# Performance work log

Measured on AMD Instinct MI355X. Metric: run time of the kernel, lower is better.

Reference implementation:

```python
import jax, jax.numpy as jnp
import numpy as np

FLOW_NUM = 2048
H = 64  # lstm_output_dim
NOISE_DIM = 3


def _w(key, shape, s=0.08):
    return (jax.random.normal(key, shape, dtype=jnp.float32) * s)


def setup_inputs() -> dict:
    key = jax.random.key(0)
    ks = jax.random.split(key, 20)
    d = {
        "noise": jax.random.normal(ks[0], (FLOW_NUM, NOISE_DIM), dtype=jnp.float32),
        "w_ih0": _w(ks[1], (4 * H, NOISE_DIM)),
        "w_hh0": _w(ks[2], (4 * H, H)),
        "b_ih0": _w(ks[3], (4 * H,)),
        "b_hh0": _w(ks[4], (4 * H,)),
        "w_ih1": _w(ks[5], (4 * H, H)),
        "w_hh1": _w(ks[6], (4 * H, H)),
        "b_ih1": _w(ks[7], (4 * H,)),
        "b_hh1": _w(ks[8], (4 * H,)),
        "w_ih2": _w(ks[9], (4 * H, H)),
        "w_hh2": _w(ks[10], (4 * H, H)),
        "b_ih2": _w(ks[11], (4 * H,)),
        "b_hh2": _w(ks[12], (4 * H,)),
        "fc1_w": _w(ks[13], (32, H)),
        "fc1_b": _w(ks[14], (32,)),
        "fc2_w": _w(ks[15], (16, 32)),
        "fc2_b": _w(ks[16], (16,)),
        "fc3_w": _w(ks[17], (3, 16)),
        "fc3_b": _w(ks[18], (3,)),
        "flow_length": 500,
    }
    return d


def _lstm_cell(x, h, c, w_ih, w_hh, b_ih, b_hh):
    # PyTorch gate order: input, forget, cell(g), output
    gates = x @ w_ih.T + h @ w_hh.T + (b_ih + b_hh)
    i, f, g, o = jnp.split(gates, 4, axis=-1)
    c_new = jax.nn.sigmoid(f) * c + jax.nn.sigmoid(i) * jnp.tanh(g)
    h_new = jax.nn.sigmoid(o) * jnp.tanh(c_new)
    return h_new, c_new


def reference(noise, w_ih0, w_hh0, b_ih0, b_hh0,
              w_ih1, w_hh1, b_ih1, b_hh1,
              w_ih2, w_hh2, b_ih2, b_hh2,
              fc1_w, fc1_b, fc2_w, fc2_b, fc3_w, fc3_b,
              flow_length):
    layers = [(w_ih0, w_hh0, b_ih0, b_hh0),
              (w_ih1, w_hh1, b_ih1, b_hh1),
              (w_ih2, w_hh2, b_ih2, b_hh2)]
    n = noise.shape[0]
    h0 = jnp.zeros((3, n, H), dtype=noise.dtype)
    c0 = jnp.zeros((3, n, H), dtype=noise.dtype)

    def step(carry, _):
        x, h, c = carry
        inp = x
        hs, cs = [], []
        for l, (wi, wh, bi, bh) in enumerate(layers):
            h_l, c_l = _lstm_cell(inp, h[l], c[l], wi, wh, bi, bh)
            hs.append(h_l)
            cs.append(c_l)
            inp = h_l
        # MLP head (Dropout is identity in eval mode); LeakyReLU slope 0.01
        y = jax.nn.leaky_relu(inp @ fc1_w.T + fc1_b)
        y = jax.nn.leaky_relu(y @ fc2_w.T + fc2_b)
        y = jax.nn.leaky_relu(y @ fc3_w.T + fc3_b)
        return (y, jnp.stack(hs), jnp.stack(cs)), y

    _, flow = jax.lax.scan(step, (noise, h0, c0), None, length=flow_length)
    # flow: [flow_length, flow_num, 3] -> [flow_num, flow_length, 3]
    return jnp.swapaxes(flow, 0, 1)
```

## Files before the change

### kernel.cpp

```cpp
#include <hip/hip_runtime.h>

#define NT 512

typedef _Float16 f16x8 __attribute__((ext_vector_type(8)));
typedef _Float16 f16x4 __attribute__((ext_vector_type(4)));
typedef float    f32x4 __attribute__((ext_vector_type(4)));

#define MFMA(a, b, c) __builtin_amdgcn_mfma_f32_16x16x32_f16((a), (b), (c), 0, 0, 0)

#if __has_builtin(__builtin_amdgcn_exp2f)
__device__ __forceinline__ float fexp(float x) { return __builtin_amdgcn_exp2f(x * 1.4426950408889634f); }
#else
__device__ __forceinline__ float fexp(float x) { return __expf(x); }
#endif
#if __has_builtin(__builtin_amdgcn_rcpf)
__device__ __forceinline__ float frcp(float x) { return __builtin_amdgcn_rcpf(x); }
#else
__device__ __forceinline__ float frcp(float x) { return 1.0f / x; }
#endif
__device__ __forceinline__ float sigm(float x)  { return frcp(1.0f + fexp(-x)); }
__device__ __forceinline__ float tanh_(float x) { return 1.0f - 2.0f * frcp(1.0f + fexp(2.0f * x)); }
__device__ __forceinline__ float lrelu(float x) { return x > 0.0f ? x : 0.01f * x; }

__device__ __forceinline__ f16x8 ld8(const float* p) {
    const float4* q = (const float4*)p;
    float4 a = q[0], b = q[1];
    f16x8 r = { (_Float16)a.x, (_Float16)a.y, (_Float16)a.z, (_Float16)a.w,
                (_Float16)b.x, (_Float16)b.y, (_Float16)b.z, (_Float16)b.w };
    return r;
}

__device__ __forceinline__ f16x8 zero8() {
    f16x8 z;
#pragma unroll
    for (int i = 0; i < 8; ++i) z[i] = (_Float16)0.0f;
    return z;
}

__global__ __launch_bounds__(NT, 2)
void gen_kernel(
    const float* __restrict__ noise,
    const float* __restrict__ w_ih0, const float* __restrict__ w_hh0,
    const float* __restrict__ b_ih0, const float* __restrict__ b_hh0,
    const float* __restrict__ w_ih1, const float* __restrict__ w_hh1,
    const float* __restrict__ b_ih1, const float* __restrict__ b_hh1,
    const float* __restrict__ w_ih2, const float* __restrict__ w_hh2,
    const float* __restrict__ b_ih2, const float* __restrict__ b_hh2,
    const float* __restrict__ fc1_w, const float* __restrict__ fc1_b,
    const float* __restrict__ fc2_w, const float* __restrict__ fc2_b,
    const float* __restrict__ fc3_w, const float* __restrict__ fc3_b,
    const int*   __restrict__ flow_len_p,
    float* __restrict__ out)
{
    __shared__ _Float16 sh[3][16 * 64] __attribute__((aligned(16)));
    __shared__ _Float16 sy1[8][16][40] __attribute__((aligned(16)));
    __shared__ _Float16 sy2[8][16][40] __attribute__((aligned(16)));

    const int tid  = threadIdx.x;
    const int l    = tid & 63;
    const int w    = tid >> 6;
    const int ls   = l & 15;
    const int lj   = l >> 4;
    const int base = blockIdx.x * 8;
    const int T    = flow_len_p[0];

    const int gA  = ls & 3;
    const int rA0 = gA * 64 + 4 * (2 * w + 0) + (ls >> 2);
    const int rA1 = gA * 64 + 4 * (2 * w + 1) + (ls >> 2);

    f16x8 A1[2][4], A2[2][4], A0[2][3];
#pragma unroll
    for (int kc = 0; kc < 2; ++kc) {
        A1[0][kc]     = ld8(w_ih1 + rA0 * 64 + 32 * kc + 8 * lj);
        A1[1][kc]     = ld8(w_ih1 + rA1 * 64 + 32 * kc + 8 * lj);
        A1[0][2 + kc] = ld8(w_hh1 + rA0 * 64 + 32 * kc + 8 * lj);
        A1[1][2 + kc] = ld8(w_hh1 + rA1 * 64 + 32 * kc + 8 * lj);
        A2[0][kc]     = ld8(w_ih2 + rA0 * 64 + 32 * kc + 8 * lj);
        A2[1][kc]     = ld8(w_ih2 + rA1 * 64 + 32 * kc + 8 * lj);
        A2[0][2 + kc] = ld8(w_hh2 + rA0 * 64 + 32 * kc + 8 * lj);
        A2[1][2 + kc] = ld8(w_hh2 + rA1 * 64 + 32 * kc + 8 * lj);
        A0[0][kc]     = ld8(w_hh0 + rA0 * 64 + 32 * kc + 8 * lj);
        A0[1][kc]     = ld8(w_hh0 + rA1 * 64 + 32 * kc + 8 * lj);
    }
#pragma unroll
    for (int tt = 0; tt < 2; ++tt) {
        const int r = tt ? rA1 : rA0;
        f16x8 v;
#pragma unroll
        for (int i = 0; i < 8; ++i) {
            int kl = 8 * lj + i;
            float x = (kl < 3) ? w_ih0[r * 3 + kl]
                    : (kl == 3) ? (b_ih0[r] + b_hh0[r]) : 0.0f;
            v[i] = (_Float16)x;
        }
        A0[tt][2] = v;
    }
    f16x8 F1[2][2], F2, F3;
#pragma unroll
    for (int tt = 0; tt < 2; ++tt)
#pragma unroll
        for (int kc = 0; kc < 2; ++kc)
            F1[tt][kc] = ld8(fc1_w + (16 * tt + ls) * 64 + 32 * kc + 8 * lj);
    F2 = ld8(fc2_w + ls * 32 + 8 * lj);
    {
        f16x8 v;
#pragma unroll
        for (int i = 0; i < 8; ++i) {
            int k = 8 * lj + i;
            v[i] = (_Float16)((ls < 3 && k < 16) ? fc3_w[ls * 16 + k] : 0.0f);
        }
        F3 = v;
    }
    const int uc0 = 8 * w + lj, uc1 = 8 * w + 4 + lj;
    const int u_own = (ls < 8) ? uc0 : uc1;
    const int cs    = ls & 7;
    const int whaddr = cs * 64 + 8 * (((u_own >> 3) + cs) & 7) + (u_own & 7);
    float b1o[4], b2o[4];
#pragma unroll
    for (int g = 0; g < 4; ++g) {
        b1o[g] = b_ih1[g * 64 + u_own] + b_hh1[g * 64 + u_own];
        b2o[g] = b_ih2[g * 64 + u_own] + b_hh2[g * 64 + u_own];
    }
    float hb1a[4], hb1b[4], hb2[4];
#pragma unroll
    for (int r = 0; r < 4; ++r) {
        hb1a[r] = fc1_b[4 * lj + r];
        hb1b[r] = fc1_b[16 + 4 * lj + r];
        hb2[r]  = fc2_b[4 * lj + r];
    }
    float fb3[3] = { fc3_b[0], fc3_b[1], fc3_b[2] };

    for (int i = tid; i < 3 * 16 * 64; i += NT) ((_Float16*)sh)[i] = (_Float16)0.0f;
    for (int i = tid; i < 8 * 16 * 40; i += NT) {
        ((_Float16*)sy1)[i] = (_Float16)0.0f;
        ((_Float16*)sy2)[i] = (_Float16)0.0f;
    }
    __syncthreads();

    float c0s = 0.0f, c1s = 0.0f, c2s = 0.0f;
    const float zb[4] = {0, 0, 0, 0};

#define RD(L, kg) (*(const f16x8*)&sh[L][ls * 64 + 8 * (((kg) + ls) & 7)])

#define REPACK(cell, a0, a1)                                                   \
    float cell[4];                                                             \
    _Pragma("unroll")                                                          \
    for (int r = 0; r < 4; ++r) {                                              \
        float v_ = __shfl_xor(a1[r], 8);                                       \
        cell[r] = (ls < 8) ? a0[r] : v_;                                       \
    }

#define ACTC(cell, bo, cref, L) {                                              \
        float gi = cell[0] + bo[0], gf = cell[1] + bo[1];                      \
        float gg = cell[2] + bo[2], go = cell[3] + bo[3];                      \
        cref = sigm(gf) * cref + sigm(gi) * tanh_(gg);                         \
        sh[L][whaddr] = (_Float16)(sigm(go) * tanh_(cref)); }

    {
        f16x8 bx0 = zero8();
        if (lj == 0) {
            float n0 = 0.0f, n1 = 0.0f, n2 = 0.0f;
            if (ls < 8) {
                const float* np = noise + (size_t)(base + ls) * 3;
                n0 = np[0]; n1 = np[1]; n2 = np[2];
            }
            bx0[0] = (_Float16)n0; bx0[1] = (_Float16)n1;
            bx0[2] = (_Float16)n2; bx0[3] = (_Float16)1.0f;
        }
        f32x4 a0 = {0, 0, 0, 0}, a1 = {0, 0, 0, 0};
        a0 = MFMA(A0[0][2], bx0, a0);
        a1 = MFMA(A0[1][2], bx0, a1);
        REPACK(cell, a0, a1)
        ACTC(cell, zb, c0s, 0)
    }
    f16x8 h1r0 = zero8(), h1r1 = zero8();
    f16x8 h2r0 = zero8(), h2r1 = zero8();
    __syncthreads();

    for (int t = 0; t < T; ++t) {
        f16x8 r0 = RD(0, lj), r1 = RD(0, 4 + lj);
        {
            f32x4 u0 = {0,0,0,0}, u1 = {0,0,0,0}, v0 = {0,0,0,0}, v1 = {0,0,0,0};
            v0 = MFMA(A1[0][2], h1r0, v0); v1 = MFMA(A1[1][2], h1r0, v1);
            v0 = MFMA(A1[0][3], h1r1, v0); v1 = MFMA(A1[1][3], h1r1, v1);
            u0 = MFMA(A1[0][0], r0, u0);   u1 = MFMA(A1[1][0], r0, u1);
            u0 = MFMA(A1[0][1], r1, u0);   u1 = MFMA(A1[1][1], r1, u1);
            f32x4 a0 = u0 + v0, a1 = u1 + v1;
            REPACK(cell, a0, a1)
            ACTC(cell, b1o, c1s, 1)
        }
        __syncthreads();
        h1r0 = RD(1, lj); h1r1 = RD(1, 4 + lj);
        {
            f32x4 u0 = {0,0,0,0}, u1 = {0,0,0,0}, v0 = {0,0,0,0}, v1 = {0,0,0,0};
            v0 = MFMA(A2[0][2], h2r0, v0); v1 = MFMA(A2[1][2], h2r0, v1);
            v0 = MFMA(A2[0][3], h2r1, v0); v1 = MFMA(A2[1][3], h2r1, v1);
            u0 = MFMA(A2[0][0], h1r0, u0); u1 = MFMA(A2[1][0], h1r0, u1);
            u0 = MFMA(A2[0][1], h1r1, u0); u1 = MFMA(A2[1][1], h1r1, u1);
            f32x4 a0 = u0 + v0, a1 = u1 + v1;
            REPACK(cell, a0, a1)
            ACTC(cell, b2o, c2s, 2)
        }
        __syncthreads();
        h2r0 = RD(2, lj); h2r1 = RD(2, 4 + lj);
        {
            f32x4 h0a = {0,0,0,0}, h0b = {0,0,0,0};
            h0a = MFMA(A0[0][0], r0, h0a); h0b = MFMA(A0[1][0], r0, h0b);
            h0a = MFMA(A0[0][1], r1, h0a); h0b = MFMA(A0[1][1], r1, h0b);
            f32x4 y1a = {0,0,0,0}, y1b = {0,0,0,0};
            y1a = MFMA(F1[0][0], h2r0, y1a); y1b = MFMA(F1[1][0], h2r0, y1b);
            y1a = MFMA(F1[0][1], h2r1, y1a); y1b = MFMA(F1[1][1], h2r1, y1b);
            f16x4 vv;
#pragma unroll
            for (int r = 0; r < 4; ++r) vv[r] = (_Float16)lrelu(y1a[r] + hb1a[r]);
            *(f16x4*)&sy1[w][ls][4 * lj] = vv;
#pragma unroll
            for (int r = 0; r < 4; ++r) vv[r] = (_Float16)lrelu(y1b[r] + hb1b[r]);
            *(f16x4*)&sy1[w][ls][16 + 4 * lj] = vv;
            f16x8 by1 = *(const f16x8*)&sy1[w][ls][8 * lj];
            f32x4 y2 = {0,0,0,0};
            y2 = MFMA(F2, by1, y2);
#pragma unroll
            for (int r = 0; r < 4; ++r) vv[r] = (_Float16)lrelu(y2[r] + hb2[r]);
            *(f16x4*)&sy2[w][ls][4 * lj] = vv;
            f16x8 by2 = *(const f16x8*)&sy2[w][ls][8 * lj];
            f32x4 y3 = {0,0,0,0};
            y3 = MFMA(F3, by2, y3);
            f16x8 bx = zero8();
            if (lj == 0) {
                float o0 = lrelu(y3[0] + fb3[0]);
                float o1 = lrelu(y3[1] + fb3[1]);
                float o2 = lrelu(y3[2] + fb3[2]);
                bx[0] = (_Float16)o0; bx[1] = (_Float16)o1;
                bx[2] = (_Float16)o2; bx[3] = (_Float16)1.0f;
                if (w == 0 && ls < 8) {
                    float* op = out + ((size_t)(base + ls) * T + t) * 3;
                    op[0] = o0; op[1] = o1; op[2] = o2;
                }
            }
            h0a = MFMA(A0[0][2], bx, h0a);
            h0b = MFMA(A0[1][2], bx, h0b);
            REPACK(cell, h0a, h0b)
            ACTC(cell, zb, c0s, 0)
        }
        __syncthreads();
    }
}

extern "C" void kernel_launch(void* const* d_in, const int* in_sizes, int n_in,
                              void* d_out, int out_size, void* d_ws, size_t ws_size,
                              hipStream_t stream) {
    const float* noise = (const float*)d_in[0];
    const float* w_ih0 = (const float*)d_in[1];
    const float* w_hh0 = (const float*)d_in[2];
    const float* b_ih0 = (const float*)d_in[3];
    const float* b_hh0 = (const float*)d_in[4];
    const float* w_ih1 = (const float*)d_in[5];
    const float* w_hh1 = (const float*)d_in[6];
    const float* b_ih1 = (const float*)d_in[7];
    const float* b_hh1 = (const float*)d_in[8];
    const float* w_ih2 = (const float*)d_in[9];
    const float* w_hh2 = (const float*)d_in[10];
    const float* b_ih2 = (const float*)d_in[11];
    const float* b_hh2 = (const float*)d_in[12];
    const float* fc1w  = (const float*)d_in[13];
    const float* fc1b  = (const float*)d_in[14];
    const float* fc2w  = (const float*)d_in[15];
    const float* fc2b  = (const float*)d_in[16];
    const float* fc3w  = (const float*)d_in[17];
    const float* fc3b  = (const float*)d_in[18];
    const int*   flp   = (const int*)d_in[19];

    gen_kernel<<<dim3(256), dim3(NT), 0, stream>>>(
        noise, w_ih0, w_hh0, b_ih0, b_hh0,
        w_ih1, w_hh1, b_ih1, b_hh1,
        w_ih2, w_hh2, b_ih2, b_hh2,
        fc1w, fc1b, fc2w, fc2b, fc3w, fc3b,
        flp, (float*)d_out);
}
```

Measured before the change: 831.7 us.

## Halve block to 4 waves, each wave computing two gate-unit slices

```diff
diff --git a/kernel.cpp b/kernel.cpp
--- a/kernel.cpp
+++ b/kernel.cpp
@@ -1,6 +1,6 @@
 #include <hip/hip_runtime.h>
 
-#define NT 512
+#define NT 256
 
 typedef _Float16 f16x8 __attribute__((ext_vector_type(8)));
 typedef _Float16 f16x4 __attribute__((ext_vector_type(4)));
@@ -37,7 +37,7 @@
     return z;
 }
 
-__global__ __launch_bounds__(NT, 2)
+__global__ __launch_bounds__(NT, 1)
 void gen_kernel(
     const float* __restrict__ noise,
     const float* __restrict__ w_ih0, const float* __restrict__ w_hh0,
@@ -53,8 +53,8 @@
     float* __restrict__ out)
 {
     __shared__ _Float16 sh[3][16 * 64] __attribute__((aligned(16)));
-    __shared__ _Float16 sy1[8][16][40] __attribute__((aligned(16)));
-    __shared__ _Float16 sy2[8][16][40] __attribute__((aligned(16)));
+    __shared__ _Float16 sy1[4][16][40] __attribute__((aligned(16)));
+    __shared__ _Float16 sy2[4][16][40] __attribute__((aligned(16)));
 
     const int tid  = threadIdx.x;
     const int l    = tid & 63;
@@ -64,36 +64,27 @@
     const int base = blockIdx.x * 8;
     const int T    = flow_len_p[0];
 
-    const int gA  = ls & 3;
-    const int rA0 = gA * 64 + 4 * (2 * w + 0) + (ls >> 2);
-    const int rA1 = gA * 64 + 4 * (2 * w + 1) + (ls >> 2);
-
-    f16x8 A1[2][4], A2[2][4], A0[2][3];
-#pragma unroll
-    for (int kc = 0; kc < 2; ++kc) {
-        A1[0][kc]     = ld8(w_ih1 + rA0 * 64 + 32 * kc + 8 * lj);
-        A1[1][kc]     = ld8(w_ih1 + rA1 * 64 + 32 * kc + 8 * lj);
-        A1[0][2 + kc] = ld8(w_hh1 + rA0 * 64 + 32 * kc + 8 * lj);
-        A1[1][2 + kc] = ld8(w_hh1 + rA1 * 64 + 32 * kc + 8 * lj);
-        A2[0][kc]     = ld8(w_ih2 + rA0 * 64 + 32 * kc + 8 * lj);
-        A2[1][kc]     = ld8(w_ih2 + rA1 * 64 + 32 * kc + 8 * lj);
-        A2[0][2 + kc] = ld8(w_hh2 + rA0 * 64 + 32 * kc + 8 * lj);
-        A2[1][2 + kc] = ld8(w_hh2 + rA1 * 64 + 32 * kc + 8 * lj);
-        A0[0][kc]     = ld8(w_hh0 + rA0 * 64 + 32 * kc + 8 * lj);
-        A0[1][kc]     = ld8(w_hh0 + rA1 * 64 + 32 * kc + 8 * lj);
-    }
-#pragma unroll
-    for (int tt = 0; tt < 2; ++tt) {
-        const int r = tt ? rA1 : rA0;
+    f16x8 A1[4][4], A2[4][4], A0[4][3];
+#pragma unroll
+    for (int p = 0; p < 4; ++p) {
+        const int rA = (ls & 3) * 64 + 4 * (4 * w + p) + (ls >> 2);
+#pragma unroll
+        for (int kc = 0; kc < 2; ++kc) {
+            A1[p][kc]     = ld8(w_ih1 + rA * 64 + 32 * kc + 8 * lj);
+            A1[p][2 + kc] = ld8(w_hh1 + rA * 64 + 32 * kc + 8 * lj);
+            A2[p][kc]     = ld8(w_ih2 + rA * 64 + 32 * kc + 8 * lj);
+            A2[p][2 + kc] = ld8(w_hh2 + rA * 64 + 32 * kc + 8 * lj);
+            A0[p][kc]     = ld8(w_hh0 + rA * 64 + 32 * kc + 8 * lj);
+        }
         f16x8 v;
 #pragma unroll
         for (int i = 0; i < 8; ++i) {
             int kl = 8 * lj + i;
-            float x = (kl < 3) ? w_ih0[r * 3 + kl]
-                    : (kl == 3) ? (b_ih0[r] + b_hh0[r]) : 0.0f;
+            float x = (kl < 3) ? w_ih0[rA * 3 + kl]
+                    : (kl == 3) ? (b_ih0[rA] + b_hh0[rA]) : 0.0f;
             v[i] = (_Float16)x;
         }
-        A0[tt][2] = v;
+        A0[p][2] = v;
     }
     f16x8 F1[2][2], F2, F3;
 #pragma unroll
@@ -111,15 +102,18 @@
         }
         F3 = v;
     }
-    const int uc0 = 8 * w + lj, uc1 = 8 * w + 4 + lj;
-    const int u_own = (ls < 8) ? uc0 : uc1;
-    const int cs    = ls & 7;
-    const int whaddr = cs * 64 + 8 * (((u_own >> 3) + cs) & 7) + (u_own & 7);
-    float b1o[4], b2o[4];
+    const int u0 = 16 * w + ((ls < 8) ? 0 : 4) + lj;
+    const int u1 = u0 + 8;
+    const int cs = ls & 7;
+    const int wh0 = cs * 64 + 8 * (((u0 >> 3) + cs) & 7) + (u0 & 7);
+    const int wh1 = cs * 64 + 8 * (((u1 >> 3) + cs) & 7) + (u1 & 7);
+    float b1o0[4], b1o1[4], b2o0[4], b2o1[4];
 #pragma unroll
     for (int g = 0; g < 4; ++g) {
-        b1o[g] = b_ih1[g * 64 + u_own] + b_hh1[g * 64 + u_own];
-        b2o[g] = b_ih2[g * 64 + u_own] + b_hh2[g * 64 + u_own];
+        b1o0[g] = b_ih1[g * 64 + u0] + b_hh1[g * 64 + u0];
+        b1o1[g] = b_ih1[g * 64 + u1] + b_hh1[g * 64 + u1];
+        b2o0[g] = b_ih2[g * 64 + u0] + b_hh2[g * 64 + u0];
+        b2o1[g] = b_ih2[g * 64 + u1] + b_hh2[g * 64 + u1];
     }
     float hb1a[4], hb1b[4], hb2[4];
 #pragma unroll
@@ -131,13 +125,13 @@
     float fb3[3] = { fc3_b[0], fc3_b[1], fc3_b[2] };
 
     for (int i = tid; i < 3 * 16 * 64; i += NT) ((_Float16*)sh)[i] = (_Float16)0.0f;
-    for (int i = tid; i < 8 * 16 * 40; i += NT) {
+    for (int i = tid; i < 4 * 16 * 40; i += NT) {
         ((_Float16*)sy1)[i] = (_Float16)0.0f;
         ((_Float16*)sy2)[i] = (_Float16)0.0f;
     }
     __syncthreads();
 
-    float c0s = 0.0f, c1s = 0.0f, c2s = 0.0f;
+    float c0a = 0.0f, c0b = 0.0f, c1a = 0.0f, c1b = 0.0f, c2a = 0.0f, c2b = 0.0f;
     const float zb[4] = {0, 0, 0, 0};
 
 #define RD(L, kg) (*(const f16x8*)&sh[L][ls * 64 + 8 * (((kg) + ls) & 7)])
@@ -150,11 +144,11 @@
         cell[r] = (ls < 8) ? a0[r] : v_;                                       \
     }
 
-#define ACTC(cell, bo, cref, L) {                                              \
+#define ACTC(cell, bo, cref, L, wa) {                                          \
         float gi = cell[0] + bo[0], gf = cell[1] + bo[1];                      \
         float gg = cell[2] + bo[2], go = cell[3] + bo[3];                      \
         cref = sigm(gf) * cref + sigm(gi) * tanh_(gg);                         \
-        sh[L][whaddr] = (_Float16)(sigm(go) * tanh_(cref)); }
+        sh[L][wa] = (_Float16)(sigm(go) * tanh_(cref)); }
 
     {
         f16x8 bx0 = zero8();
@@ -167,11 +161,11 @@
             bx0[0] = (_Float16)n0; bx0[1] = (_Float16)n1;
             bx0[2] = (_Float16)n2; bx0[3] = (_Float16)1.0f;
         }
-        f32x4 a0 = {0, 0, 0, 0}, a1 = {0, 0, 0, 0};
-        a0 = MFMA(A0[0][2], bx0, a0);
-        a1 = MFMA(A0[1][2], bx0, a1);
-        REPACK(cell, a0, a1)
-        ACTC(cell, zb, c0s, 0)
+        f32x4 g0 = {0,0,0,0}, g1 = {0,0,0,0}, g2 = {0,0,0,0}, g3 = {0,0,0,0};
+        g0 = MFMA(A0[0][2], bx0, g0); g1 = MFMA(A0[1][2], bx0, g1);
+        g2 = MFMA(A0[2][2], bx0, g2); g3 = MFMA(A0[3][2], bx0, g3);
+        REPACK(cell0, g0, g1) ACTC(cell0, zb, c0a, 0, wh0)
+        REPACK(cell1, g2, g3) ACTC(cell1, zb, c0b, 0, wh1)
     }
     f16x8 h1r0 = zero8(), h1r1 = zero8();
     f16x8 h2r0 = zero8(), h2r1 = zero8();
@@ -180,33 +174,41 @@
     for (int t = 0; t < T; ++t) {
         f16x8 r0 = RD(0, lj), r1 = RD(0, 4 + lj);
         {
-            f32x4 u0 = {0,0,0,0}, u1 = {0,0,0,0}, v0 = {0,0,0,0}, v1 = {0,0,0,0};
-            v0 = MFMA(A1[0][2], h1r0, v0); v1 = MFMA(A1[1][2], h1r0, v1);
-            v0 = MFMA(A1[0][3], h1r1, v0); v1 = MFMA(A1[1][3], h1r1, v1);
-            u0 = MFMA(A1[0][0], r0, u0);   u1 = MFMA(A1[1][0], r0, u1);
-            u0 = MFMA(A1[0][1], r1, u0);   u1 = MFMA(A1[1][1], r1, u1);
-            f32x4 a0 = u0 + v0, a1 = u1 + v1;
-            REPACK(cell, a0, a1)
-            ACTC(cell, b1o, c1s, 1)
+            f32x4 g0 = {0,0,0,0}, g1 = {0,0,0,0}, g2 = {0,0,0,0}, g3 = {0,0,0,0};
+            g0 = MFMA(A1[0][2], h1r0, g0); g1 = MFMA(A1[1][2], h1r0, g1);
+            g2 = MFMA(A1[2][2], h1r0, g2); g3 = MFMA(A1[3][2], h1r0, g3);
+            g0 = MFMA(A1[0][3], h1r1, g0); g1 = MFMA(A1[1][3], h1r1, g1);
+            g2 = MFMA(A1[2][3], h1r1, g2); g3 = MFMA(A1[3][3], h1r1, g3);
+            g0 = MFMA(A1[0][0], r0, g0);   g1 = MFMA(A1[1][0], r0, g1);
+            g2 = MFMA(A1[2][0], r0, g2);   g3 = MFMA(A1[3][0], r0, g3);
+            g0 = MFMA(A1[0][1], r1, g0);   g1 = MFMA(A1[1][1], r1, g1);
+            g2 = MFMA(A1[2][1], r1, g2);   g3 = MFMA(A1[3][1], r1, g3);
+            REPACK(cell0, g0, g1) ACTC(cell0, b1o0, c1a, 1, wh0)
+            REPACK(cell1, g2, g3) ACTC(cell1, b1o1, c1b, 1, wh1)
         }
         __syncthreads();
         h1r0 = RD(1, lj); h1r1 = RD(1, 4 + lj);
         {
-            f32x4 u0 = {0,0,0,0}, u1 = {0,0,0,0}, v0 = {0,0,0,0}, v1 = {0,0,0,0};
-            v0 = MFMA(A2[0][2], h2r0, v0); v1 = MFMA(A2[1][2], h2r0, v1);
-            v0 = MFMA(A2[0][3], h2r1, v0); v1 = MFMA(A2[1][3], h2r1, v1);
-            u0 = MFMA(A2[0][0], h1r0, u0); u1 = MFMA(A2[1][0], h1r0, u1);
-            u0 = MFMA(A2[0][1], h1r1, u0); u1 = MFMA(A2[1][1], h1r1, u1);
-            f32x4 a0 = u0 + v0, a1 = u1 + v1;
-            REPACK(cell, a0, a1)
-            ACTC(cell, b2o, c2s, 2)
+            f32x4 g0 = {0,0,0,0}, g1 = {0,0,0,0}, g2 = {0,0,0,0}, g3 = {0,0,0,0};
+            g0 = MFMA(A2[0][2], h2r0, g0); g1 = MFMA(A2[1][2], h2r0, g1);
+            g2 = MFMA(A2[2][2], h2r0, g2); g3 = MFMA(A2[3][2], h2r0, g3);
+            g0 = MFMA(A2[0][3], h2r1, g0); g1 = MFMA(A2[1][3], h2r1, g1);
+            g2 = MFMA(A2[2][3], h2r1, g2); g3 = MFMA(A2[3][3], h2r1, g3);
+            g0 = MFMA(A2[0][0], h1r0, g0); g1 = MFMA(A2[1][0], h1r0, g1);
+            g2 = MFMA(A2[2][0], h1r0, g2); g3 = MFMA(A2[3][0], h1r0, g3);
+            g0 = MFMA(A2[0][1], h1r1, g0); g1 = MFMA(A2[1][1], h1r1, g1);
+            g2 = MFMA(A2[2][1], h1r1, g2); g3 = MFMA(A2[3][1], h1r1, g3);
+            REPACK(cell0, g0, g1) ACTC(cell0, b2o0, c2a, 2, wh0)
+            REPACK(cell1, g2, g3) ACTC(cell1, b2o1, c2b, 2, wh1)
         }
         __syncthreads();
         h2r0 = RD(2, lj); h2r1 = RD(2, 4 + lj);
         {
-            f32x4 h0a = {0,0,0,0}, h0b = {0,0,0,0};
-            h0a = MFMA(A0[0][0], r0, h0a); h0b = MFMA(A0[1][0], r0, h0b);
-            h0a = MFMA(A0[0][1], r1, h0a); h0b = MFMA(A0[1][1], r1, h0b);
+            f32x4 h0g0 = {0,0,0,0}, h0g1 = {0,0,0,0}, h0g2 = {0,0,0,0}, h0g3 = {0,0,0,0};
+            h0g0 = MFMA(A0[0][0], r0, h0g0); h0g1 = MFMA(A0[1][0], r0, h0g1);
+            h0g2 = MFMA(A0[2][0], r0, h0g2); h0g3 = MFMA(A0[3][0], r0, h0g3);
+            h0g0 = MFMA(A0[0][1], r1, h0g0); h0g1 = MFMA(A0[1][1], r1, h0g1);
+            h0g2 = MFMA(A0[2][1], r1, h0g2); h0g3 = MFMA(A0[3][1], r1, h0g3);
             f32x4 y1a = {0,0,0,0}, y1b = {0,0,0,0};
             y1a = MFMA(F1[0][0], h2r0, y1a); y1b = MFMA(F1[1][0], h2r0, y1b);
             y1a = MFMA(F1[0][1], h2r1, y1a); y1b = MFMA(F1[1][1], h2r1, y1b);
@@ -238,10 +240,10 @@
                     op[0] = o0; op[1] = o1; op[2] = o2;
                 }
             }
-            h0a = MFMA(A0[0][2], bx, h0a);
-            h0b = MFMA(A0[1][2], bx, h0b);
-            REPACK(cell, h0a, h0b)
-            ACTC(cell, zb, c0s, 0)
+            h0g0 = MFMA(A0[0][2], bx, h0g0); h0g1 = MFMA(A0[1][2], bx, h0g1);
+            h0g2 = MFMA(A0[2][2], bx, h0g2); h0g3 = MFMA(A0[3][2], bx, h0g3);
+            REPACK(cell0, h0g0, h0g1) ACTC(cell0, zb, c0a, 0, wh0)
+            REPACK(cell1, h0g2, h0g3) ACTC(cell1, zb, c0b, 0, wh1)
         }
         __syncthreads();
     }
```

Result: slower. 942.7 us (+13.3%).
